# Kernel optimization log

Measured on AMD Instinct MI355X. Metric: run time of the kernel, lower is better.

The kernel has to match this reference:

```python
import jax, jax.numpy as jnp
import numpy as np

# Faithful JAX port of the approxmatch algorithm (Fan et al. / PyTorch-EMDLoss CUDA kernel):
# iterative soft bipartite matching with annealed temperature levels -4^j for j=8..-1, then 0,
# tracking remaining capacities ('saturation') of both point sets.

EPS = 1e-9

def _approx_match(xyz1, xyz2):
    # xyz1: [B,N,D], xyz2: [B,M,D] -> match: [B,N,M]
    B, n, _ = xyz1.shape
    m = xyz2.shape[1]
    factorl = max(n, m) // n  # capacity per point in set 1
    factorr = max(n, m) // m  # capacity per point in set 2
    # pairwise squared distances [B,N,M]
    d2 = jnp.sum((xyz1[:, :, None, :] - xyz2[:, None, :, :]) ** 2, axis=-1)
    # annealing levels: -4^8, -4^7, ..., -4^-1, 0
    levels = jnp.array([-(4.0 ** j) for j in range(8, -2, -1)] + [0.0],
                       dtype=xyz1.dtype)
    satl0 = jnp.full((B, n), float(factorl), dtype=xyz1.dtype)
    satr0 = jnp.full((B, m), float(factorr), dtype=xyz1.dtype)
    match0 = jnp.zeros((B, n, m), dtype=xyz1.dtype)

    def step(carry, level):
        satl, satr, match = carry
        # soft assignment weights scaled by remaining capacity of set 2
        w = jnp.exp(level * d2) * satr[:, None, :]                      # [B,N,M]
        # row-normalize, scaled by remaining capacity of set 1
        w = w / (jnp.sum(w, axis=2, keepdims=True) + EPS) * satl[:, :, None]
        # column capacity clipping
        ss = jnp.sum(w, axis=1) + EPS                                   # [B,M]
        r = jnp.minimum(satr / ss, 1.0)
        w = w * r[:, None, :]
        satr = jnp.maximum(satr - jnp.sum(w, axis=1), 0.0)
        satl = jnp.maximum(satl - jnp.sum(w, axis=2), 0.0)
        return (satl, satr, match + w), None

    (_, _, match), _ = jax.lax.scan(step, (satl0, satr0, match0), levels)
    return match


def setup_inputs() -> dict:
    key = jax.random.key(0)
    k1, k2 = jax.random.split(key)
    xyz1 = jax.random.normal(k1, (8, 2048, 3), dtype=jnp.float32)
    xyz2 = jax.random.normal(k2, (8, 2048, 3), dtype=jnp.float32)
    return {"xyz1": xyz1, "xyz2": xyz2}


def reference(xyz1, xyz2):
    # EMD cost per batch element: sum_{k,l} match[k,l] * ||x1_k - x2_l||
    match = _approx_match(xyz1, xyz2)                                   # [B,N,M]
    d = jnp.sqrt(jnp.sum((xyz1[:, :, None, :] - xyz2[:, None, :, :]) ** 2,
                         axis=-1))                                      # [B,N,M]
    return jnp.sum(match * d, axis=(1, 2))                              # [B]
```

## Files before the change

kernel.cpp:

```cpp
#include <hip/hip_runtime.h>
#include <math.h>

static constexpr int   B_   = 8;
static constexpr int   N_   = 2048;
static constexpr int   TPB  = 256;
static constexpr int   TILE = 32;
static constexpr int   NBLK = (B_ * N_) / TILE;
static constexpr int   BN   = B_ * N_;
static constexpr float EPS_ = 1e-9f;

#define WS_X1    (ws)
#define WS_X2    (ws + 4*BN)
#define WS_SATL  (ws + 8*BN)
#define WS_SATR  (ws + 9*BN)
#define WS_SCAL  (ws + 10*BN)
#define WS_LSCAL (ws + 11*BN)
#define WS_LSATR (ws + 12*BN)
#define WS_WR    (ws + 13*BN)
#define WS_LWR   (ws + 14*BN)
#define WS_COST  (ws + 15*BN)

__global__ void __launch_bounds__(TPB)
emd_init(const float* __restrict__ xyz1, const float* __restrict__ xyz2,
         float* __restrict__ ws)
{
    const int idx = blockIdx.x * TPB + threadIdx.x;
    if (idx >= BN) return;
    float x = xyz1[idx*3], y = xyz1[idx*3+1], z = xyz1[idx*3+2];
    reinterpret_cast<float4*>(WS_X1)[idx] =
        make_float4(x, y, z, fmaf(x,x, fmaf(y,y, z*z)));
    x = xyz2[idx*3]; y = xyz2[idx*3+1]; z = xyz2[idx*3+2];
    reinterpret_cast<float4*>(WS_X2)[idx] =
        make_float4(x, y, z, fmaf(x,x, fmaf(y,y, z*z)));
    WS_SATL[idx] = 1.f;
    WS_SATR[idx] = 1.f;
    WS_LSATR[idx] = 0.f;
    WS_COST[idx] = 0.f;
}

template<int MODE>
__global__ void __launch_bounds__(TPB)
emd_pass(float* __restrict__ ws, const float lvlA, const float lvlB)
{
    __shared__ float4 pts[N_];
    __shared__ float  auxA[N_];
    __shared__ float  auxB[N_];
    __shared__ float  red[64][33];

    const int b    = blockIdx.x >> 6;
    const int tile = blockIdx.x & 63;
    const int t    = threadIdx.x;
    const int g    = t & 3;
    const int c    = t >> 2;

    const float4* src = (MODE == 1)
        ? reinterpret_cast<const float4*>(WS_X1) + b * N_
        : reinterpret_cast<const float4*>(WS_X2) + b * N_;
    const float* aA = (MODE == 0) ? (WS_LSATR + b * N_)
                     : (MODE == 1) ? (WS_LSCAL + b * N_)
                     : (MODE == 2) ? (WS_LWR   + b * N_)
                                   : (WS_WR    + b * N_);
    const float* aB = WS_LSATR + b * N_;
    for (int p = t; p < N_; p += TPB) {
        pts[p]  = src[p];
        auxA[p] = aA[p];
        if (MODE == 2) auxB[p] = aB[p];
    }

    const float4* ownv = (MODE == 1)
        ? reinterpret_cast<const float4*>(WS_X2)
        : reinterpret_cast<const float4*>(WS_X1);
    const int obase = b * N_ + tile * TILE + g * 8;
    float cx[8], cy[8], cz[8], cq[8];
#pragma unroll
    for (int j = 0; j < 8; ++j) {
        float4 v = ownv[obase + j];
        cx[j] = -2.f * v.x; cy[j] = -2.f * v.y; cz[j] = -2.f * v.z;
        cq[j] = v.w;
    }
    __syncthreads();

    float s1[8], s2[8], s3[8];
#pragma unroll
    for (int j = 0; j < 8; ++j) { s1[j] = 0.f; s2[j] = 0.f; s3[j] = 0.f; }

    for (int i = 0; i < 32; ++i) {
        const int l = c + (i << 6);
        const float4 p = pts[l];
        const float  wA = auxA[l];
        float wB;
        if (MODE == 2) wB = auxB[l];
#pragma unroll
        for (int j = 0; j < 8; ++j) {
            const float s0 = p.w + cq[j];
            const float d2 = fmaf(cx[j], p.x,
                             fmaf(cy[j], p.y,
                             fmaf(cz[j], p.z, s0)));
            if (MODE == 0 || MODE == 1) {
                s1[j] += __builtin_amdgcn_exp2f(fmaf(lvlB, d2, wA));
            } else if (MODE == 2) {
                const float sq = __builtin_amdgcn_sqrtf(fmaxf(d2, 0.f));
                const float eA = __builtin_amdgcn_exp2f(fmaf(lvlA, d2, wA));
                s1[j] += eA;
                s2[j]  = fmaf(eA, sq, s2[j]);
                s3[j] += __builtin_amdgcn_exp2f(fmaf(lvlB, d2, wB));
            } else {
                const float sq = __builtin_amdgcn_sqrtf(fmaxf(d2, 0.f));
                s2[j] = fmaf(wA, sq, s2[j]);
            }
        }
    }

    float rs1 = 0.f, rs2 = 0.f, rs3 = 0.f;
    if (MODE != 3) {
#pragma unroll
        for (int j = 0; j < 8; ++j) red[c][g * 8 + j] = s1[j];
        __syncthreads();
        if (t < TILE) for (int cc = 0; cc < 64; ++cc) rs1 += red[cc][t];
    }
    if (MODE >= 2) {
        if (MODE != 3) __syncthreads();
#pragma unroll
        for (int j = 0; j < 8; ++j) red[c][g * 8 + j] = s2[j];
        __syncthreads();
        if (t < TILE) for (int cc = 0; cc < 64; ++cc) rs2 += red[cc][t];
    }
    if (MODE == 2) {
        __syncthreads();
#pragma unroll
        for (int j = 0; j < 8; ++j) red[c][g * 8 + j] = s3[j];
        __syncthreads();
        if (t < TILE) for (int cc = 0; cc < 64; ++cc) rs3 += red[cc][t];
    }

    if (t < TILE) {
        const int idx = b * N_ + tile * TILE + t;
        if (MODE == 0) {
            const float sc = WS_SATL[idx] / (rs1 + EPS_);
            WS_SCAL[idx]  = sc;
            WS_LSCAL[idx] = __log2f(sc);
        } else if (MODE == 1) {
            const float sr  = WS_SATR[idx];
            const float w1s = sr * rs1;
            const float rr  = fminf(sr / (w1s + EPS_), 1.f);
            const float wrv = sr * rr;
            const float srn = fmaxf(sr - rr * w1s, 0.f);
            WS_WR[idx]    = wrv;
            WS_LWR[idx]   = __log2f(wrv);
            WS_SATR[idx]  = srn;
            WS_LSATR[idx] = __log2f(srn);
        } else if (MODE == 2) {
            const float scp  = WS_SCAL[idx];
            const float sln  = fmaxf(WS_SATL[idx] - scp * rs1, 0.f);
            WS_COST[idx]     = fmaf(scp, rs2, WS_COST[idx]);
            const float scn  = sln / (rs3 + EPS_);
            WS_SATL[idx]  = sln;
            WS_SCAL[idx]  = scn;
            WS_LSCAL[idx] = __log2f(scn);
        } else {
            WS_COST[idx] = fmaf(WS_SCAL[idx], rs2, WS_COST[idx]);
        }
    }
}

__global__ void __launch_bounds__(TPB)
emd_finish(const float* __restrict__ cost, float* __restrict__ out)
{
    const int b = blockIdx.x;
    const int t = threadIdx.x;
    float v = 0.f;
    for (int i = t; i < N_; i += TPB) v += cost[b * N_ + i];
#pragma unroll
    for (int k = 32; k >= 1; k >>= 1) v += __shfl_xor(v, k, 64);
    __shared__ float wsum[4];
    if ((t & 63) == 0) wsum[t >> 6] = v;
    __syncthreads();
    if (t == 0) out[b] = wsum[0] + wsum[1] + wsum[2] + wsum[3];
}

extern "C" void kernel_launch(void* const* d_in, const int* in_sizes, int n_in,
                              void* d_out, int out_size, void* d_ws, size_t ws_size,
                              hipStream_t stream)
{
    const float* xyz1 = (const float*)d_in[0];
    const float* xyz2 = (const float*)d_in[1];
    float* out = (float*)d_out;
    float* ws  = (float*)d_ws;

    emd_init<<<BN / TPB, TPB, 0, stream>>>(xyz1, xyz2, ws);

    static const float levels[11] = {
        -65536.f, -16384.f, -4096.f, -1024.f, -256.f,
        -64.f, -16.f, -4.f, -1.f, -0.25f, 0.f};
    const float LOG2E = 1.4426950408889634f;

    emd_pass<0><<<NBLK, TPB, 0, stream>>>(ws, 0.f, levels[0] * LOG2E);
    emd_pass<1><<<NBLK, TPB, 0, stream>>>(ws, 0.f, levels[0] * LOG2E);
    for (int lev = 1; lev < 11; ++lev) {
        emd_pass<2><<<NBLK, TPB, 0, stream>>>(ws, levels[lev-1] * LOG2E,
                                                  levels[lev]   * LOG2E);
        emd_pass<1><<<NBLK, TPB, 0, stream>>>(ws, 0.f, levels[lev] * LOG2E);
    }
    emd_pass<3><<<NBLK, TPB, 0, stream>>>(ws, 0.f, 0.f);

    emd_finish<<<B_, TPB, 0, stream>>>(WS_COST, out);
}
```

Baseline: 352.3 us.

## Fold level scaling into precomputed coordinates, pack aux data, tree-reduce, prefetch loop

Moves the level multiply into the per-point constants: the own-point coordinates are prescaled by -2*level and the staged w component becomes level*|p|^2 plus the log weight, so modes 0 and 1 compute the exponent argument with three FMAs and no separate scale. Merges LWR and LSATR into one float2 array, reuses the point buffer's shared memory for the reduction, and sets occupancy hints through launch_bounds. Replaces the serial 64-step column reduction with a two-level tree and software-prefetches the next point in the inner loops. Mode 3 also reduces cost per block so the final kernel only sums 64 partials per batch. Folding the scale into the constants changes floating-point rounding in the large-magnitude exponent arguments, which may shift accuracy at the steepest annealing levels.

```diff
diff --git a/kernel.cpp b/kernel.cpp
--- a/kernel.cpp
+++ b/kernel.cpp
@@ -8,6 +8,7 @@
 static constexpr int   NBLK = (B_ * N_) / TILE;
 static constexpr int   BN   = B_ * N_;
 static constexpr float EPS_ = 1e-9f;
+static constexpr float LOG2E = 1.4426950408889634f;
 
 #define WS_X1    (ws)
 #define WS_X2    (ws + 4*BN)
@@ -15,10 +16,10 @@
 #define WS_SATR  (ws + 9*BN)
 #define WS_SCAL  (ws + 10*BN)
 #define WS_LSCAL (ws + 11*BN)
-#define WS_LSATR (ws + 12*BN)
-#define WS_WR    (ws + 13*BN)
-#define WS_LWR   (ws + 14*BN)
+#define WS_WLS   (reinterpret_cast<float2*>(ws + 12*BN))
+#define WS_WR    (ws + 14*BN)
 #define WS_COST  (ws + 15*BN)
+#define WS_COSTP (ws + 16*BN)
 
 __global__ void __launch_bounds__(TPB)
 emd_init(const float* __restrict__ xyz1, const float* __restrict__ xyz2,
@@ -34,18 +35,20 @@
         make_float4(x, y, z, fmaf(x,x, fmaf(y,y, z*z)));
     WS_SATL[idx] = 1.f;
     WS_SATR[idx] = 1.f;
-    WS_LSATR[idx] = 0.f;
     WS_COST[idx] = 0.f;
+    WS_WLS[idx]  = make_float2(0.f, 0.f);
 }
 
 template<int MODE>
-__global__ void __launch_bounds__(TPB)
+__global__ void __launch_bounds__(TPB, (MODE == 2) ? 3 : 4)
 emd_pass(float* __restrict__ ws, const float lvlA, const float lvlB)
 {
-    __shared__ float4 pts[N_];
-    __shared__ float  auxA[N_];
-    __shared__ float  auxB[N_];
-    __shared__ float  red[64][33];
+    constexpr int SMEM_BYTES = (MODE == 2) ? (32768 + 16384) : 32768;
+    __shared__ __align__(16) char smem[SMEM_BYTES];
+    float4* pts  = reinterpret_cast<float4*>(smem);
+    float2* aux2 = reinterpret_cast<float2*>(smem + 32768);
+    float (*red)[33]  = reinterpret_cast<float(*)[33]>(smem);
+    float (*red2)[33] = reinterpret_cast<float(*)[33]>(smem + 64*33*4);
 
     const int b    = blockIdx.x >> 6;
     const int tile = blockIdx.x & 63;
@@ -53,30 +56,46 @@
     const int g    = t & 3;
     const int c    = t >> 2;
 
-    const float4* src = (MODE == 1)
-        ? reinterpret_cast<const float4*>(WS_X1) + b * N_
-        : reinterpret_cast<const float4*>(WS_X2) + b * N_;
-    const float* aA = (MODE == 0) ? (WS_LSATR + b * N_)
-                     : (MODE == 1) ? (WS_LSCAL + b * N_)
-                     : (MODE == 2) ? (WS_LWR   + b * N_)
-                                   : (WS_WR    + b * N_);
-    const float* aB = WS_LSATR + b * N_;
+    const float4* x1v = reinterpret_cast<const float4*>(WS_X1) + b * N_;
+    const float4* x2v = reinterpret_cast<const float4*>(WS_X2) + b * N_;
+    const float2* wls = WS_WLS + b * N_;
+    const float*  lscal = WS_LSCAL + b * N_;
+    const float*  wrp   = WS_WR + b * N_;
+
     for (int p = t; p < N_; p += TPB) {
-        pts[p]  = src[p];
-        auxA[p] = aA[p];
-        if (MODE == 2) auxB[p] = aB[p];
-    }
-
-    const float4* ownv = (MODE == 1)
-        ? reinterpret_cast<const float4*>(WS_X2)
-        : reinterpret_cast<const float4*>(WS_X1);
-    const int obase = b * N_ + tile * TILE + g * 8;
-    float cx[8], cy[8], cz[8], cq[8];
+        if (MODE == 0) {
+            float4 v = x2v[p];
+            pts[p] = make_float4(v.x, v.y, v.z, fmaf(lvlB, v.w, wls[p].y));
+        } else if (MODE == 1) {
+            float4 v = x1v[p];
+            pts[p] = make_float4(v.x, v.y, v.z, fmaf(lvlB, v.w, lscal[p]));
+        } else if (MODE == 2) {
+            float4 v = x2v[p];
+            pts[p] = v;
+            float2 q = wls[p];
+            aux2[p] = make_float2(fmaf(lvlA, v.w, q.x), fmaf(lvlB, v.w, q.y));
+        } else {
+            float4 v = x2v[p];
+            pts[p] = make_float4(v.x, v.y, v.z, wrp[p]);
+        }
+    }
+
+    const float4* ownv = (MODE == 1) ? x2v : x1v;
+    const int ob = tile * TILE + g * 8;
+    float kx[8], ky[8], kz[8], kq[8];
 #pragma unroll
     for (int j = 0; j < 8; ++j) {
-        float4 v = ownv[obase + j];
-        cx[j] = -2.f * v.x; cy[j] = -2.f * v.y; cz[j] = -2.f * v.z;
-        cq[j] = v.w;
+        float4 v = ownv[ob + j];
+        if (MODE == 0 || MODE == 1) {
+            const float m2lv = -2.f * lvlB;
+            kx[j] = m2lv * v.x; ky[j] = m2lv * v.y; kz[j] = m2lv * v.z;
+            kq[j] = lvlB * v.w;
+        } else if (MODE == 2) {
+            kx[j] = -2.f * v.x; ky[j] = -2.f * v.y; kz[j] = -2.f * v.z;
+            kq[j] = v.w;
+        } else {
+            kx[j] = v.x; ky[j] = v.y; kz[j] = v.z; kq[j] = 0.f;
+        }
     }
     __syncthreads();
 
@@ -84,98 +103,130 @@
 #pragma unroll
     for (int j = 0; j < 8; ++j) { s1[j] = 0.f; s2[j] = 0.f; s3[j] = 0.f; }
 
-    for (int i = 0; i < 32; ++i) {
-        const int l = c + (i << 6);
-        const float4 p = pts[l];
-        const float  wA = auxA[l];
-        float wB;
-        if (MODE == 2) wB = auxB[l];
-#pragma unroll
-        for (int j = 0; j < 8; ++j) {
-            const float s0 = p.w + cq[j];
-            const float d2 = fmaf(cx[j], p.x,
-                             fmaf(cy[j], p.y,
-                             fmaf(cz[j], p.z, s0)));
-            if (MODE == 0 || MODE == 1) {
-                s1[j] += __builtin_amdgcn_exp2f(fmaf(lvlB, d2, wA));
-            } else if (MODE == 2) {
+    int l = c;
+    float4 p = pts[l];
+    float2 a;
+    if (MODE == 2) a = aux2[l];
+
+    if (MODE == 0 || MODE == 1) {
+#pragma unroll 4
+        for (int i = 0; i < 32; ++i) {
+            const int ln = (l + 64) & (N_ - 1);
+            const float4 pn = pts[ln];
+#pragma unroll
+            for (int j = 0; j < 8; ++j) {
+                const float arg = fmaf(kx[j], p.x, fmaf(ky[j], p.y,
+                                  fmaf(kz[j], p.z, p.w + kq[j])));
+                s1[j] += __builtin_amdgcn_exp2f(arg);
+            }
+            p = pn; l = ln;
+        }
+    } else if (MODE == 2) {
+#pragma unroll 2
+        for (int i = 0; i < 32; ++i) {
+            const int ln = (l + 64) & (N_ - 1);
+            const float4 pn = pts[ln];
+            const float2 an = aux2[ln];
+#pragma unroll
+            for (int j = 0; j < 8; ++j) {
+                const float dq = fmaf(kx[j], p.x, fmaf(ky[j], p.y,
+                                 fmaf(kz[j], p.z, kq[j])));
+                const float d2 = p.w + dq;
                 const float sq = __builtin_amdgcn_sqrtf(fmaxf(d2, 0.f));
-                const float eA = __builtin_amdgcn_exp2f(fmaf(lvlA, d2, wA));
+                const float eA = __builtin_amdgcn_exp2f(fmaf(lvlA, dq, a.x));
+                const float eB = __builtin_amdgcn_exp2f(fmaf(lvlB, dq, a.y));
                 s1[j] += eA;
                 s2[j]  = fmaf(eA, sq, s2[j]);
-                s3[j] += __builtin_amdgcn_exp2f(fmaf(lvlB, d2, wB));
-            } else {
+                s3[j] += eB;
+            }
+            p = pn; a = an; l = ln;
+        }
+    } else {
+#pragma unroll 4
+        for (int i = 0; i < 32; ++i) {
+            const int ln = (l + 64) & (N_ - 1);
+            const float4 pn = pts[ln];
+#pragma unroll
+            for (int j = 0; j < 8; ++j) {
+                const float dx = p.x - kx[j], dy = p.y - ky[j], dz = p.z - kz[j];
+                const float d2 = fmaf(dx, dx, fmaf(dy, dy, dz * dz));
                 const float sq = __builtin_amdgcn_sqrtf(fmaxf(d2, 0.f));
-                s2[j] = fmaf(wA, sq, s2[j]);
+                s2[j] = fmaf(p.w, sq, s2[j]);
             }
-        }
-    }
-
-    float rs1 = 0.f, rs2 = 0.f, rs3 = 0.f;
-    if (MODE != 3) {
-#pragma unroll
-        for (int j = 0; j < 8; ++j) red[c][g * 8 + j] = s1[j];
-        __syncthreads();
-        if (t < TILE) for (int cc = 0; cc < 64; ++cc) rs1 += red[cc][t];
-    }
-    if (MODE >= 2) {
-        if (MODE != 3) __syncthreads();
-#pragma unroll
-        for (int j = 0; j < 8; ++j) red[c][g * 8 + j] = s2[j];
-        __syncthreads();
-        if (t < TILE) for (int cc = 0; cc < 64; ++cc) rs2 += red[cc][t];
-    }
-    if (MODE == 2) {
-        __syncthreads();
-#pragma unroll
-        for (int j = 0; j < 8; ++j) red[c][g * 8 + j] = s3[j];
-        __syncthreads();
-        if (t < TILE) for (int cc = 0; cc < 64; ++cc) rs3 += red[cc][t];
-    }
-
-    if (t < TILE) {
-        const int idx = b * N_ + tile * TILE + t;
-        if (MODE == 0) {
-            const float sc = WS_SATL[idx] / (rs1 + EPS_);
-            WS_SCAL[idx]  = sc;
-            WS_LSCAL[idx] = __log2f(sc);
-        } else if (MODE == 1) {
-            const float sr  = WS_SATR[idx];
+            p = pn; l = ln;
+        }
+    }
+
+#define REDUCE(arr, dst)                                                   \
+    {   __syncthreads();                                                   \
+        _Pragma("unroll")                                                  \
+        for (int j = 0; j < 8; ++j) red[c][g * 8 + j] = arr[j];            \
+        __syncthreads();                                                   \
+        { const int o = t & 31, sg = t >> 5; float a2 = 0.f;               \
+          _Pragma("unroll")                                                \
+          for (int k = 0; k < 8; ++k) a2 += red[sg * 8 + k][o];            \
+          red2[sg][o] = a2; }                                              \
+        __syncthreads();                                                   \
+        dst = 0.f;                                                         \
+        if (t < TILE) { _Pragma("unroll")                                  \
+            for (int sgg = 0; sgg < 8; ++sgg) dst += red2[sgg][t]; } }
+
+    const int gidx = b * N_ + tile * TILE + t;
+
+    if (MODE == 0) {
+        float rs1; REDUCE(s1, rs1);
+        if (t < TILE) {
+            const float sc = WS_SATL[gidx] / (rs1 + EPS_);
+            WS_SCAL[gidx]  = sc;
+            WS_LSCAL[gidx] = __log2f(sc);
+        }
+    } else if (MODE == 1) {
+        float rs1; REDUCE(s1, rs1);
+        if (t < TILE) {
+            const float sr  = WS_SATR[gidx];
             const float w1s = sr * rs1;
             const float rr  = fminf(sr / (w1s + EPS_), 1.f);
             const float wrv = sr * rr;
             const float srn = fmaxf(sr - rr * w1s, 0.f);
-            WS_WR[idx]    = wrv;
-            WS_LWR[idx]   = __log2f(wrv);
-            WS_SATR[idx]  = srn;
-            WS_LSATR[idx] = __log2f(srn);
-        } else if (MODE == 2) {
-            const float scp  = WS_SCAL[idx];
-            const float sln  = fmaxf(WS_SATL[idx] - scp * rs1, 0.f);
-            WS_COST[idx]     = fmaf(scp, rs2, WS_COST[idx]);
-            const float scn  = sln / (rs3 + EPS_);
-            WS_SATL[idx]  = sln;
-            WS_SCAL[idx]  = scn;
-            WS_LSCAL[idx] = __log2f(scn);
-        } else {
-            WS_COST[idx] = fmaf(WS_SCAL[idx], rs2, WS_COST[idx]);
-        }
-    }
-}
-
-__global__ void __launch_bounds__(TPB)
-emd_finish(const float* __restrict__ cost, float* __restrict__ out)
+            WS_SATR[gidx] = srn;
+            WS_WR[gidx]   = wrv;
+            WS_WLS[gidx + b * N_ * 0] = make_float2(__log2f(wrv), __log2f(srn));
+        }
+    } else if (MODE == 2) {
+        float rs1, rs2, rs3;
+        REDUCE(s1, rs1); REDUCE(s2, rs2); REDUCE(s3, rs3);
+        if (t < TILE) {
+            const float scp = WS_SCAL[gidx];
+            const float sln = fmaxf(WS_SATL[gidx] - scp * rs1, 0.f);
+            WS_COST[gidx]   = fmaf(scp, rs2, WS_COST[gidx]);
+            const float scn = sln / (rs3 + EPS_);
+            WS_SATL[gidx]  = sln;
+            WS_SCAL[gidx]  = scn;
+            WS_LSCAL[gidx] = __log2f(scn);
+        }
+    } else {
+        float rs2; REDUCE(s2, rs2);
+        float v = 0.f;
+        if (t < TILE)
+            v = fmaf(WS_SCAL[gidx], rs2, WS_COST[gidx]);
+        if (t < 64) {
+#pragma unroll
+            for (int k = 16; k >= 1; k >>= 1) v += __shfl_xor(v, k, 64);
+            if (t == 0) WS_COSTP[blockIdx.x] = v;
+        }
+    }
+#undef REDUCE
+}
+
+__global__ void __launch_bounds__(64)
+emd_finish(const float* __restrict__ costp, float* __restrict__ out)
 {
     const int b = blockIdx.x;
     const int t = threadIdx.x;
-    float v = 0.f;
-    for (int i = t; i < N_; i += TPB) v += cost[b * N_ + i];
+    float v = costp[b * 64 + t];
 #pragma unroll
     for (int k = 32; k >= 1; k >>= 1) v += __shfl_xor(v, k, 64);
-    __shared__ float wsum[4];
-    if ((t & 63) == 0) wsum[t >> 6] = v;
-    __syncthreads();
-    if (t == 0) out[b] = wsum[0] + wsum[1] + wsum[2] + wsum[3];
+    if (t == 0) out[b] = v;
 }
 
 extern "C" void kernel_launch(void* const* d_in, const int* in_sizes, int n_in,
@@ -192,7 +243,6 @@
     static const float levels[11] = {
         -65536.f, -16384.f, -4096.f, -1024.f, -256.f,
         -64.f, -16.f, -4.f, -1.f, -0.25f, 0.f};
-    const float LOG2E = 1.4426950408889634f;
 
     emd_pass<0><<<NBLK, TPB, 0, stream>>>(ws, 0.f, levels[0] * LOG2E);
     emd_pass<1><<<NBLK, TPB, 0, stream>>>(ws, 0.f, levels[0] * LOG2E);
@@ -203,5 +253,5 @@
     }
     emd_pass<3><<<NBLK, TPB, 0, stream>>>(ws, 0.f, 0.f);
 
-    emd_finish<<<B_, TPB, 0, stream>>>(WS_COST, out);
-}
+    emd_finish<<<B_, 64, 0, stream>>>(WS_COSTP, out);
+}
```

After: 339.2 us. 3.7% less time.
